# Kernel tuning notes

Measured on AMD Instinct MI355X. Metric: run time of the kernel, lower is better.

## Reference

```python
import jax, jax.numpy as jnp
import numpy as np

N_NODES = 50000
N_EDGES = 800000
N_RELS = 8
IN_FEATS = 128
OUT_FEATS = 128


def setup_inputs() -> dict:
    key = jax.random.key(0)
    k = jax.random.split(key, 7)
    stdv = 1.0 / np.sqrt(IN_FEATS)
    return {
        "h": jax.random.normal(k[0], (N_NODES, IN_FEATS), dtype=jnp.float32),
        "edge_norm": jax.random.uniform(k[1], (N_EDGES,), dtype=jnp.float32),
        "edge_types": jax.random.randint(k[2], (N_EDGES,), 0, N_RELS, dtype=jnp.int32),
        "src": jax.random.randint(k[3], (N_EDGES,), 0, N_NODES, dtype=jnp.int32),
        "dst": jax.random.randint(k[4], (N_EDGES,), 0, N_NODES, dtype=jnp.int32),
        "weight": jax.random.uniform(k[5], (N_RELS, IN_FEATS, OUT_FEATS), jnp.float32, -stdv, stdv),
        "bias": jax.random.uniform(k[6], (OUT_FEATS,), jnp.float32, -stdv, stdv),
    }


def reference(h, edge_norm, edge_types, src, dst, weight, bias):
    # Per-relation dense transform: [N, R, O]
    ht = jnp.einsum("ni,rio->nro", h, weight)
    # Gather transformed src feature under each edge's relation, scale by edge norm
    msg = ht[src, edge_types] * edge_norm[:, None]  # [E, O]
    # Scatter-sum messages to destination nodes
    out = jax.ops.segment_sum(msg, dst, num_segments=h.shape[0])  # [N, O]
    out = out + bias
    return jax.nn.relu(out)
```

## Files before the change

kernel.cpp:

```cpp
#include <hip/hip_runtime.h>
#include <hip/hip_bf16.h>

#define N_NODES 50000
#define N_EDGES 800000
#define N_RELS  8
#define NKEYS   400000
#define NTOT    400384
#define NB1     1564

typedef __attribute__((ext_vector_type(8))) short bf16x8;
typedef __attribute__((ext_vector_type(4))) float f32x4;

typedef const __attribute__((address_space(1))) unsigned int* gptr_t;
typedef __attribute__((address_space(3))) unsigned int* lptr_t;

__device__ __forceinline__ unsigned short f2b(float f) {
    unsigned int u = __float_as_uint(f);
    u += 0x7fffu + ((u >> 16) & 1u);
    return (unsigned short)(u >> 16);
}

__global__ void prep_kernel(const float* __restrict__ h, unsigned short* __restrict__ hb,
                            const float* __restrict__ w, unsigned short* __restrict__ wt2,
                            const int* __restrict__ dst, const int* __restrict__ et,
                            int* __restrict__ counts2) {
    int b = blockIdx.x;
    if (b < 6250) {
        int i = b * 256 + threadIdx.x;
        float4 v = ((const float4*)h)[i];
        ushort4 o;
        o.x = f2b(v.x); o.y = f2b(v.y); o.z = f2b(v.z); o.w = f2b(v.w);
        ((ushort4*)hb)[i] = o;
    } else if (b < 6762) {
        int idx = (b - 6250) * 256 + threadIdx.x;
        int r = idx >> 14;
        int k = (idx >> 7) & 127;
        int o = idx & 127;
        int off = (r << 14) + ((o >> 4) << 11) + ((k >> 3) << 7) + ((o & 15) << 3) + (k & 7);
        wt2[off] = f2b(w[idx]);
    } else {
        int e = (b - 6762) * 256 + threadIdx.x;
        atomicAdd(&counts2[dst[e] * 8 + et[e]], 1);
    }
}

__global__ __launch_bounds__(256) void lbscan_kernel(int* __restrict__ counts,
                                                     unsigned long long* __restrict__ status,
                                                     int* __restrict__ row_start2) {
    __shared__ int tmp[256];
    __shared__ int s_exc;
    const int b = blockIdx.x;
    const int tid = threadIdx.x;
    const int i = b * 256 + tid;
    int v = counts[i];
    tmp[tid] = v;
    __syncthreads();
    #pragma unroll
    for (int off = 1; off < 256; off <<= 1) {
        int t = (tid >= off) ? tmp[tid - off] : 0;
        __syncthreads();
        tmp[tid] += t;
        __syncthreads();
    }
    int inc = tmp[tid];
    int btot = tmp[255];
    if (tid == 0) {
        unsigned long long st = (b == 0) ? ((2ULL << 32) | (unsigned)btot)
                                         : ((1ULL << 32) | (unsigned)btot);
        atomicExch(&status[b], st);
        if (b == 0) s_exc = 0;
    }
    if (b > 0 && tid < 64) {
        int lane = tid;
        int exc = 0;
        int base = b - 64;
        while (true) {
            int j = base + lane;
            unsigned flag = 2u; unsigned val = 0u;
            if (j >= 0) {
                unsigned long long st;
                do { st = atomicAdd(&status[j], 0ULL); flag = (unsigned)(st >> 32); } while (flag == 0u);
                val = (unsigned)st;
            }
            unsigned long long pmask = __ballot(flag == 2u);
            int contrib;
            int done = (pmask != 0ULL);
            if (done) {
                int p = 63 - __clzll(pmask);
                contrib = (lane >= p) ? (int)val : 0;
            } else {
                contrib = (int)val;
            }
            #pragma unroll
            for (int s = 1; s < 64; s <<= 1) contrib += __shfl_xor(contrib, s);
            exc += contrib;
            if (done) break;
            base -= 64;
        }
        if (lane == 0) {
            s_exc = exc;
            atomicExch(&status[b], (2ULL << 32) | (unsigned)(exc + btot));
        }
    }
    __syncthreads();
    int rs = s_exc + inc - v;
    if (i <= NKEYS) row_start2[i] = rs;
    if (i < NKEYS) counts[i] = rs;
}

__global__ void scatter_kernel(const int* __restrict__ src, const int* __restrict__ dst,
                               const int* __restrict__ et, const float* __restrict__ en,
                               int* __restrict__ cursor2, int2* __restrict__ meta) {
    int e = blockIdx.x * 256 + threadIdx.x;
    int key = dst[e] * 8 + et[e];
    int pos = atomicAdd(&cursor2[key], 1);
    meta[pos] = make_int2(src[e] << 8, __float_as_int(en[e]));
}

__global__ __launch_bounds__(256) void agg_kernel(const char* __restrict__ hb,
                                                  const int2* __restrict__ meta,
                                                  const int* __restrict__ row_start2,
                                                  char* __restrict__ agg) {
    int node = blockIdx.x * 4 + (threadIdx.x >> 6);
    int lane = threadIdx.x & 63;
    int rs[9];
    #pragma unroll
    for (int r = 0; r < 9; ++r) rs[r] = row_start2[node * 8 + r];

    float2 acc[N_RELS];
    #pragma unroll
    for (int r = 0; r < N_RELS; ++r) acc[r] = make_float2(0.f, 0.f);

    for (int base = rs[0]; base < rs[8]; base += 64) {
        int hi = rs[8] < base + 64 ? rs[8] : base + 64;
        int2 m = make_int2(0, 0);
        if (base + lane < rs[8]) m = meta[base + lane];
        #pragma unroll
        for (int r = 0; r < N_RELS; ++r) {
            int ks = (rs[r] > base ? rs[r] : base) - base;
            int ke = (rs[r + 1] < hi ? rs[r + 1] : hi) - base;
            int k = ks;
            for (; k + 2 <= ke; k += 2) {
                int o0 = __builtin_amdgcn_readlane(m.x, k);
                float w0 = __uint_as_float(__builtin_amdgcn_readlane(m.y, k));
                int o1 = __builtin_amdgcn_readlane(m.x, k + 1);
                float w1 = __uint_as_float(__builtin_amdgcn_readlane(m.y, k + 1));
                unsigned int v0 = *(const unsigned int*)(hb + o0 + lane * 4);
                unsigned int v1 = *(const unsigned int*)(hb + o1 + lane * 4);
                acc[r].x += __uint_as_float(v0 << 16) * w0;
                acc[r].y += __uint_as_float(v0 & 0xffff0000u) * w0;
                acc[r].x += __uint_as_float(v1 << 16) * w1;
                acc[r].y += __uint_as_float(v1 & 0xffff0000u) * w1;
            }
            if (k < ke) {
                int o0 = __builtin_amdgcn_readlane(m.x, k);
                float w0 = __uint_as_float(__builtin_amdgcn_readlane(m.y, k));
                unsigned int v0 = *(const unsigned int*)(hb + o0 + lane * 4);
                acc[r].x += __uint_as_float(v0 << 16) * w0;
                acc[r].y += __uint_as_float(v0 & 0xffff0000u) * w0;
            }
        }
    }
    int sw = (((lane >> 2) ^ (node & 15)) << 4) + (lane & 3) * 4;
    #pragma unroll
    for (int r = 0; r < N_RELS; ++r) {
        unsigned int u = (unsigned int)f2b(acc[r].x) | ((unsigned int)f2b(acc[r].y) << 16);
        *(unsigned int*)(agg + ((size_t)(r * 50048 + node)) * 256 + sw) = u;
    }
}

__global__ __launch_bounds__(256) void gemm2_kernel(const char* __restrict__ agg,
                                                    const char* __restrict__ wt2,
                                                    const float* __restrict__ bias,
                                                    float* __restrict__ out) {
    __shared__ char Ws[32768];
    __shared__ char Bs[16384];
    const int n0 = blockIdx.x * 64;
    const int tid = threadIdx.x;
    const int wave = tid >> 6, lane = tid & 63;
    const int m16 = lane & 15, quad = lane >> 4;

    f32x4 acc[8];
    #pragma unroll
    for (int og = 0; og < 8; ++og) acc[og] = (f32x4){0.f, 0.f, 0.f, 0.f};

    for (int r = 0; r < N_RELS; ++r) {
        __syncthreads();
        const char* wsrc = wt2 + ((size_t)r << 15);
        const char* bsrc = agg + ((size_t)(r * 50048 + n0)) * 256;
        #pragma unroll
        for (int j = 0; j < 8; ++j) {
            int off = j * 4096 + wave * 1024 + lane * 16;
            __builtin_amdgcn_global_load_lds((gptr_t)(wsrc + off), (lptr_t)(Ws + j * 4096 + wave * 1024), 16, 0, 0);
        }
        #pragma unroll
        for (int j = 0; j < 4; ++j) {
            int off = j * 4096 + wave * 1024 + lane * 16;
            __builtin_amdgcn_global_load_lds((gptr_t)(bsrc + off), (lptr_t)(Bs + j * 4096 + wave * 1024), 16, 0, 0);
        }
        __syncthreads();
        #pragma unroll
        for (int kk = 0; kk < 4; ++kk) {
            int c = kk * 4 + quad;
            bf16x8 b = *(const bf16x8*)(Bs + (wave * 16 + m16) * 256 + ((c ^ m16) << 4));
            #pragma unroll
            for (int og = 0; og < 8; ++og) {
                bf16x8 a = *(const bf16x8*)(Ws + og * 4096 + c * 256 + m16 * 16);
                acc[og] = __builtin_amdgcn_mfma_f32_16x16x32_bf16(a, b, acc[og], 0, 0, 0);
            }
        }
    }

    int n = n0 + wave * 16 + m16;
    if (n < N_NODES) {
        #pragma unroll
        for (int og = 0; og < 8; ++og) {
            int o = og * 16 + quad * 4;
            float4 b4 = *(const float4*)&bias[o];
            float4 v;
            v.x = fmaxf(acc[og][0] + b4.x, 0.f);
            v.y = fmaxf(acc[og][1] + b4.y, 0.f);
            v.z = fmaxf(acc[og][2] + b4.z, 0.f);
            v.w = fmaxf(acc[og][3] + b4.w, 0.f);
            *(float4*)&out[(size_t)n * 128 + o] = v;
        }
    }
}

extern "C" void kernel_launch(void* const* d_in, const int* in_sizes, int n_in,
                              void* d_out, int out_size, void* d_ws, size_t ws_size,
                              hipStream_t stream) {
    const float* h    = (const float*)d_in[0];
    const float* en   = (const float*)d_in[1];
    const int*   et   = (const int*)d_in[2];
    const int*   src  = (const int*)d_in[3];
    const int*   dst  = (const int*)d_in[4];
    const float* w    = (const float*)d_in[5];
    const float* bias = (const float*)d_in[6];
    float* out = (float*)d_out;

    char* ws = (char*)d_ws;
    unsigned short* hb  = (unsigned short*)(ws);
    unsigned short* wt2 = (unsigned short*)(ws + 12800000);
    char*           agg = ws + 13062144;
    char* sbase = ws + 115560448;
    int*  counts2    = (int*)(sbase);
    unsigned long long* status = (unsigned long long*)(sbase + 1601536);
    int*  row_start2 = (int*)(sbase + 1614336);
    int2* meta       = (int2*)(sbase + 3214592);

    (void)hipMemsetAsync(counts2, 0, NTOT * sizeof(int) + NB1 * sizeof(unsigned long long), stream);
    hipLaunchKernelGGL(prep_kernel, dim3(9887), dim3(256), 0, stream, h, hb, w, wt2, dst, et, counts2);
    hipLaunchKernelGGL(lbscan_kernel, dim3(NB1), dim3(256), 0, stream, counts2, status, row_start2);
    hipLaunchKernelGGL(scatter_kernel, dim3(N_EDGES / 256), dim3(256), 0, stream, src, dst, et, en, counts2, meta);
    hipLaunchKernelGGL(agg_kernel, dim3(12500), dim3(256), 0, stream, (const char*)hb, meta, row_start2, agg);
    hipLaunchKernelGGL(gemm2_kernel, dim3(782), dim3(256), 0, stream, (const char*)agg, (const char*)wt2, bias, out);
}
```

Measured before the change: 255.3 us.

## Pack edge metadata into 32 bits with fp16 norm, vectorize scatter

Edge metadata is packed into one int: the src index goes in the upper 16 bits and edge_norm as fp16 in the lower 16. This halves the metadata written by scatter and read by aggregation. The scatter kernel now handles four edges per thread using vector loads, and aggregation splits its accumulators into two chains to add ILP. Risks: src indices up to 49999 do not fit in 16 bits as a signed shift, though they may survive as unsigned after the >>16. Rounding the norm to fp16 also costs some precision.

```diff
diff --git a/kernel.cpp b/kernel.cpp
--- a/kernel.cpp
+++ b/kernel.cpp
@@ -1,5 +1,6 @@
 #include <hip/hip_runtime.h>
 #include <hip/hip_bf16.h>
+#include <hip/hip_fp16.h>
 
 #define N_NODES 50000
 #define N_EDGES 800000
@@ -108,17 +109,30 @@
     if (i < NKEYS) counts[i] = rs;
 }
 
-__global__ void scatter_kernel(const int* __restrict__ src, const int* __restrict__ dst,
-                               const int* __restrict__ et, const float* __restrict__ en,
-                               int* __restrict__ cursor2, int2* __restrict__ meta) {
-    int e = blockIdx.x * 256 + threadIdx.x;
-    int key = dst[e] * 8 + et[e];
-    int pos = atomicAdd(&cursor2[key], 1);
-    meta[pos] = make_int2(src[e] << 8, __float_as_int(en[e]));
+__global__ __launch_bounds__(256) void scatter_kernel(const int* __restrict__ src,
+                                                      const int* __restrict__ dst,
+                                                      const int* __restrict__ et,
+                                                      const float* __restrict__ en,
+                                                      int* __restrict__ cursor2,
+                                                      int* __restrict__ meta) {
+    int t = blockIdx.x * 256 + threadIdx.x;
+    if (t >= N_EDGES / 4) return;
+    int4   d4 = ((const int4*)dst)[t];
+    int4   e4 = ((const int4*)et)[t];
+    int4   s4 = ((const int4*)src)[t];
+    float4 n4 = ((const float4*)en)[t];
+    int p0 = atomicAdd(&cursor2[d4.x * 8 + e4.x], 1);
+    int p1 = atomicAdd(&cursor2[d4.y * 8 + e4.y], 1);
+    int p2 = atomicAdd(&cursor2[d4.z * 8 + e4.z], 1);
+    int p3 = atomicAdd(&cursor2[d4.w * 8 + e4.w], 1);
+    meta[p0] = (s4.x << 16) | __half_as_ushort(__float2half_rn(n4.x));
+    meta[p1] = (s4.y << 16) | __half_as_ushort(__float2half_rn(n4.y));
+    meta[p2] = (s4.z << 16) | __half_as_ushort(__float2half_rn(n4.z));
+    meta[p3] = (s4.w << 16) | __half_as_ushort(__float2half_rn(n4.w));
 }
 
 __global__ __launch_bounds__(256) void agg_kernel(const char* __restrict__ hb,
-                                                  const int2* __restrict__ meta,
+                                                  const int* __restrict__ meta,
                                                   const int* __restrict__ row_start2,
                                                   char* __restrict__ agg) {
     int node = blockIdx.x * 4 + (threadIdx.x >> 6);
@@ -127,13 +141,13 @@
     #pragma unroll
     for (int r = 0; r < 9; ++r) rs[r] = row_start2[node * 8 + r];
 
-    float2 acc[N_RELS];
-    #pragma unroll
-    for (int r = 0; r < N_RELS; ++r) acc[r] = make_float2(0.f, 0.f);
+    float2 accA[N_RELS], accB[N_RELS];
+    #pragma unroll
+    for (int r = 0; r < N_RELS; ++r) { accA[r] = make_float2(0.f, 0.f); accB[r] = make_float2(0.f, 0.f); }
 
     for (int base = rs[0]; base < rs[8]; base += 64) {
         int hi = rs[8] < base + 64 ? rs[8] : base + 64;
-        int2 m = make_int2(0, 0);
+        int m = 0;
         if (base + lane < rs[8]) m = meta[base + lane];
         #pragma unroll
         for (int r = 0; r < N_RELS; ++r) {
@@ -141,30 +155,32 @@
             int ke = (rs[r + 1] < hi ? rs[r + 1] : hi) - base;
             int k = ks;
             for (; k + 2 <= ke; k += 2) {
-                int o0 = __builtin_amdgcn_readlane(m.x, k);
-                float w0 = __uint_as_float(__builtin_amdgcn_readlane(m.y, k));
-                int o1 = __builtin_amdgcn_readlane(m.x, k + 1);
-                float w1 = __uint_as_float(__builtin_amdgcn_readlane(m.y, k + 1));
-                unsigned int v0 = *(const unsigned int*)(hb + o0 + lane * 4);
-                unsigned int v1 = *(const unsigned int*)(hb + o1 + lane * 4);
-                acc[r].x += __uint_as_float(v0 << 16) * w0;
-                acc[r].y += __uint_as_float(v0 & 0xffff0000u) * w0;
-                acc[r].x += __uint_as_float(v1 << 16) * w1;
-                acc[r].y += __uint_as_float(v1 & 0xffff0000u) * w1;
+                unsigned m0 = (unsigned)__builtin_amdgcn_readlane(m, k);
+                unsigned m1 = (unsigned)__builtin_amdgcn_readlane(m, k + 1);
+                float w0 = __half2float(__ushort_as_half((unsigned short)(m0 & 0xffffu)));
+                float w1 = __half2float(__ushort_as_half((unsigned short)(m1 & 0xffffu)));
+                unsigned v0 = *(const unsigned int*)(hb + ((m0 >> 16) << 8) + lane * 4);
+                unsigned v1 = *(const unsigned int*)(hb + ((m1 >> 16) << 8) + lane * 4);
+                accA[r].x += __uint_as_float(v0 << 16) * w0;
+                accA[r].y += __uint_as_float(v0 & 0xffff0000u) * w0;
+                accB[r].x += __uint_as_float(v1 << 16) * w1;
+                accB[r].y += __uint_as_float(v1 & 0xffff0000u) * w1;
             }
             if (k < ke) {
-                int o0 = __builtin_amdgcn_readlane(m.x, k);
-                float w0 = __uint_as_float(__builtin_amdgcn_readlane(m.y, k));
-                unsigned int v0 = *(const unsigned int*)(hb + o0 + lane * 4);
-                acc[r].x += __uint_as_float(v0 << 16) * w0;
-                acc[r].y += __uint_as_float(v0 & 0xffff0000u) * w0;
+                unsigned m0 = (unsigned)__builtin_amdgcn_readlane(m, k);
+                float w0 = __half2float(__ushort_as_half((unsigned short)(m0 & 0xffffu)));
+                unsigned v0 = *(const unsigned int*)(hb + ((m0 >> 16) << 8) + lane * 4);
+                accA[r].x += __uint_as_float(v0 << 16) * w0;
+                accA[r].y += __uint_as_float(v0 & 0xffff0000u) * w0;
             }
         }
     }
     int sw = (((lane >> 2) ^ (node & 15)) << 4) + (lane & 3) * 4;
     #pragma unroll
     for (int r = 0; r < N_RELS; ++r) {
-        unsigned int u = (unsigned int)f2b(acc[r].x) | ((unsigned int)f2b(acc[r].y) << 16);
+        float ax = accA[r].x + accB[r].x;
+        float ay = accA[r].y + accB[r].y;
+        unsigned int u = (unsigned int)f2b(ax) | ((unsigned int)f2b(ay) << 16);
         *(unsigned int*)(agg + ((size_t)(r * 50048 + node)) * 256 + sw) = u;
     }
 }
@@ -247,12 +263,12 @@
     int*  counts2    = (int*)(sbase);
     unsigned long long* status = (unsigned long long*)(sbase + 1601536);
     int*  row_start2 = (int*)(sbase + 1614336);
-    int2* meta       = (int2*)(sbase + 3214592);
+    int*  meta       = (int*)(sbase + 3214592);
 
     (void)hipMemsetAsync(counts2, 0, NTOT * sizeof(int) + NB1 * sizeof(unsigned long long), stream);
     hipLaunchKernelGGL(prep_kernel, dim3(9887), dim3(256), 0, stream, h, hb, w, wt2, dst, et, counts2);
     hipLaunchKernelGGL(lbscan_kernel, dim3(NB1), dim3(256), 0, stream, counts2, status, row_start2);
-    hipLaunchKernelGGL(scatter_kernel, dim3(N_EDGES / 256), dim3(256), 0, stream, src, dst, et, en, counts2, meta);
+    hipLaunchKernelGGL(scatter_kernel, dim3(782), dim3(256), 0, stream, src, dst, et, en, counts2, meta);
     hipLaunchKernelGGL(agg_kernel, dim3(12500), dim3(256), 0, stream, (const char*)hb, meta, row_start2, agg);
     hipLaunchKernelGGL(gemm2_kernel, dim3(782), dim3(256), 0, stream, (const char*)agg, (const char*)wt2, bias, out);
 }
```

Measured after the change: 259.7 us. About the same (+1.7%).
